# Kernel tuning notes

Measured on AMD Instinct MI355X. Metric: run time of the kernel, lower is better.

Reference implementation:

```python
import jax, jax.numpy as jnp
import numpy as np
from jax import lax

DN = ('NCHW', 'OIHW', 'NCHW')


def _conv(x, w, b, stride, pad):
    y = lax.conv_general_dilated(x, w, (stride, stride), [(pad, pad), (pad, pad)],
                                 dimension_numbers=DN)
    return y + b[None, :, None, None]


def _deconv(x, w, b, stride, pad):
    # torch ConvTranspose2d weight: (in, out, kH, kW). Equivalent forward conv:
    # flip spatially, swap in/out, dilate input by stride, pad by k-1-pad.
    k = w.shape[2]
    kern = jnp.flip(w, (2, 3)).transpose(1, 0, 2, 3)  # (out, in, kH, kW)
    p = k - 1 - pad
    y = lax.conv_general_dilated(x, kern, (1, 1), [(p, p), (p, p)],
                                 lhs_dilation=(stride, stride), dimension_numbers=DN)
    return y + b[None, :, None, None]


def setup_inputs() -> dict:
    key = jax.random.key(0)
    ks = jax.random.split(key, 16)
    s = 0.05
    D, K, H = 64, 512, 128  # embedding_dim, num_embeddings, hidden_channels
    inp = {
        'x': jax.random.uniform(ks[0], (16, 3, 256, 256), dtype=jnp.float32),
        'conv1_w': jax.random.normal(ks[1], (H, 3, 4, 4), jnp.float32) * s,
        'conv1_b': jnp.zeros((H,), jnp.float32),
        'conv2_w': jax.random.normal(ks[2], (H, H, 4, 4), jnp.float32) * s,
        'conv2_b': jnp.zeros((H,), jnp.float32),
        'conv3_w': jax.random.normal(ks[3], (D, H, 3, 3), jnp.float32) * s,
        'conv3_b': jnp.zeros((D,), jnp.float32),
        'emb': jax.random.normal(ks[4], (K, D), jnp.float32),
        'deconv1_w': jax.random.normal(ks[5], (D, H, 4, 4), jnp.float32) * s,
        'deconv1_b': jnp.zeros((H,), jnp.float32),
        'deconv2_w': jax.random.normal(ks[6], (H, H, 4, 4), jnp.float32) * s,
        'deconv2_b': jnp.zeros((H,), jnp.float32),
        'deconv3_w': jax.random.normal(ks[7], (H, 3, 3, 3), jnp.float32) * s,
        'deconv3_b': jnp.zeros((3,), jnp.float32),
    }
    return inp


def reference(x, conv1_w, conv1_b, conv2_w, conv2_b, conv3_w, conv3_b, emb,
              deconv1_w, deconv1_b, deconv2_w, deconv2_b, deconv3_w, deconv3_b):
    # Encoder
    h = jax.nn.relu(_conv(x, conv1_w, conv1_b, 2, 1))
    h = jax.nn.relu(_conv(h, conv2_w, conv2_b, 2, 1))
    z_e = _conv(h, conv3_w, conv3_b, 1, 1)  # (B, 64, 64, 64)

    # Vector quantizer (faithful to torch: flatten NCHW directly to (-1, D))
    D = emb.shape[1]
    flat = z_e.reshape(-1, D)  # (N, D)
    d = (jnp.sum(flat * flat, axis=1, keepdims=True)
         + jnp.sum(emb * emb, axis=1)
         - 2.0 * flat @ emb.T)  # (N, K)
    indices = jnp.argmin(d, axis=1)[:, None]  # (N, 1)
    z_q = emb[indices[:, 0]].reshape(z_e.shape)

    # Decoder
    g = jax.nn.relu(_deconv(z_q, deconv1_w, deconv1_b, 2, 1))
    g = jax.nn.relu(_deconv(g, deconv2_w, deconv2_b, 2, 1))
    x_recon = jax.nn.sigmoid(_deconv(g, deconv3_w, deconv3_b, 1, 1))
    return (x_recon, indices, z_q)
```

## Files before the change

kernel.cpp:

```cpp
#include <hip/hip_runtime.h>
#include <hip/hip_bf16.h>

#define DEV __device__ __forceinline__

typedef __attribute__((ext_vector_type(8))) short bf16x8;
typedef __attribute__((ext_vector_type(4))) float f32x4;
typedef __attribute__((ext_vector_type(4))) unsigned short u16x4;

#define MFMA16(a,b,c) __builtin_amdgcn_mfma_f32_16x16x32_bf16(a,b,c,0,0,0)

DEV unsigned short bfbits(float v){ __hip_bfloat16 h = __float2bfloat16(v); return *(unsigned short*)&h; }
DEV float bf2f(unsigned short u){ __hip_bfloat16 h = *(__hip_bfloat16*)&u; return __bfloat162float(h); }
DEV void split3(float v, unsigned short& h, unsigned short& m, unsigned short& l) {
  h = bfbits(v);        float r  = v - bf2f(h);
  m = bfbits(r);        float r2 = r - bf2f(m);
  l = bfbits(r2);
}
DEV uint4 zero4(){ uint4 z; z.x=0; z.y=0; z.z=0; z.w=0; return z; }
DEV void gload_lds16(const void* g, void* l) {
  __builtin_amdgcn_global_load_lds(
      (const __attribute__((address_space(1))) void*)g,
      (__attribute__((address_space(3))) void*)l, 16, 0, 0);
}

DEV void prep_deconv_img(int i, int CI, const float* __restrict__ w, unsigned short* __restrict__ w2) {
  const int nch = CI/16;
  int cil = i & 7, s = (i >> 3) & 7, co = (i >> 6) & 127, f = (i >> 13) & 1;
  int rest = i >> 14;
  int ch = rest % nch, e = rest / nch;
  int k = ch*64 + s*8 + cil;
  int ci = (k & 15) | ((k >> 6) << 4);
  int tap = (k >> 4) & 3, a = tap >> 1, b = tap & 1;
  float v = w[ (((long)ci*128 + co)*4 + (2*a+1-e))*4 + (2*b+1-f) ];
  w2[(long)(e*nch + ch)*16384 + ((long)(f*128 + co))*64 + ((s ^ (co&7))*8) + cil] = bfbits(v);
}
__global__ __launch_bounds__(256) void wprep_all(
    const float* __restrict__ c1w, float* __restrict__ w2c1,
    const float* __restrict__ c2w, unsigned short* __restrict__ w2c2,
    const float* __restrict__ c3w, unsigned short* __restrict__ w2c3,
    const float* __restrict__ d1w, unsigned short* __restrict__ w2d1,
    const float* __restrict__ d2w, unsigned short* __restrict__ w2d2,
    const float* __restrict__ d3w, unsigned short* __restrict__ w2d3,
    const float* __restrict__ emb, float* __restrict__ esq) {
  const int bx = blockIdx.x, t = threadIdx.x;
  if (bx < 24) {
    int i = bx*256 + t;
    if (i < 6144) {
      int tap = i & 15, ci = (i>>4) % 3, co = i / 48;
      w2c1[((long)ci*16 + tap)*128 + co] = c1w[i];
    }
  } else if (bx < 1048) {
    int i = (bx-24)*256 + t;
    int cil = i & 7, s = (i>>3) & 15, co = (i>>7) & 63;
    int ch = (i>>13) & 15, cog = i >> 17;
    int co_g = cog*64 + co, ci = ch*8 + cil, ky = s >> 2, kx = s & 3;
    float v = c2w[(((long)co_g*128 + ci)*4 + ky)*4 + kx];
    unsigned short h,m,l; split3(v,h,m,l);
    long base = (long)(cog*16 + ch)*24576 + ((long)co*16 + (s ^ (co&15)))*8 + cil;
    w2c2[base] = h; w2c2[base + 8192] = m; w2c2[base + 16384] = l;
  } else if (bx < 1432) {
    int i = (bx-1048)*256 + t;
    int k = i % 1536, co = i / 1536;
    int ch = k / 96, rem = k % 96;
    int tap = rem >> 3, cil = rem & 7;
    int ci = ch*8 + cil, ky = tap >> 2, kx = tap & 3;
    float v = (kx < 3) ? c3w[(((long)co*128 + ci)*3 + ky)*3 + kx] : 0.f;
    unsigned short h,m,l; split3(v,h,m,l);
    long base = (long)ch*24576 + ((long)co*16 + (tap ^ (co&15)))*8 + cil;
    w2c3[base] = h; w2c3[base + 8192] = m; w2c3[base + 16384] = l;
  } else if (bx < 1944) {
    prep_deconv_img((bx-1432)*256 + t, 64, d1w, w2d1);
  } else if (bx < 2968) {
    prep_deconv_img((bx-1944)*256 + t, 128, d2w, w2d2);
  } else if (bx < 3064) {
    int i = (bx-2968)*256 + t;
    if (i < 24576) {
      int k = i % 1536, co = i / 1536;
      int ch = k / 96, rem = k % 96;
      int tap = rem >> 3, cil = rem & 7;
      int ci = ch*8 + cil, ky = tap >> 2, kx = tap & 3;
      float v = (co < 3 && kx < 3) ? d3w[(((long)ci*3 + co)*3 + ky)*3 + kx] : 0.f;
      w2d3[i] = bfbits(v);
    }
  } else {
    int code = (bx-3064)*256 + t;
    if (code < 512) {
      const float4* ev = (const float4*)(emb + (long)code*64);
      float s = 0.f;
      #pragma unroll
      for (int q=0;q<16;q++){ float4 e4 = ev[q];
        s += e4.x*e4.x + e4.y*e4.y + e4.z*e4.z + e4.w*e4.w; }
      esq[code] = s;
    }
  }
}

__global__ __launch_bounds__(256) void conv1_split(
    const float* __restrict__ x, const float* __restrict__ w2,
    const float* __restrict__ bias, unsigned short* __restrict__ h1, long PS1) {
  __shared__ __align__(16) float sIn[3][18][20];
  __shared__ __align__(16) float sW[3*16*64];
  const int tid = threadIdx.x;
  const int b = blockIdx.z >> 1, cog = blockIdx.z & 1;
  const int co0 = cog*64;
  const int oy0 = blockIdx.y*8, ox0 = blockIdx.x*8;
  const int cg2 = tid >> 5;
  const int pg2 = tid & 31;
  const int r = pg2 >> 2, pxp = (pg2 & 3)*2;
  float acc[8][2];
  #pragma unroll
  for (int c=0;c<8;c++){ float bv = bias[co0 + cg2*8 + c];
    acc[c][0]=bv; acc[c][1]=bv; }
  const float* xb = x + (long)b*3*256*256;
  const int iy0 = 2*oy0 - 1, ix0 = 2*ox0 - 1;
  for (int t=tid; t<3*18*18; t+=256) {
    int xx = t%18, yy=(t/18)%18, ci=t/324;
    int gy = iy0+yy, gx = ix0+xx;
    float v = 0.f;
    if (gy>=0 && gy<256 && gx>=0 && gx<256) v = xb[((long)ci*256+gy)*256+gx];
    sIn[ci][yy][xx] = v;
  }
  for (int t=tid; t<3*16*64; t+=256) {
    sW[t] = w2[(long)(t>>6)*128 + co0 + (t&63)];
  }
  __syncthreads();
  for (int ci=0; ci<3; ci++) {
    #pragma unroll
    for (int ky=0;ky<4;ky++)
    #pragma unroll
    for (int kx=0;kx<4;kx++) {
      const float* wp = &sW[(ci*16 + ky*4+kx)*64 + cg2*8];
      float4 w0 = *(const float4*)wp;
      float4 w1 = *(const float4*)(wp+4);
      const int yy = 2*r + ky;
      #pragma unroll
      for (int p=0;p<2;p++) {
        float iv = sIn[ci][yy][2*(pxp+p)+kx];
        acc[0][p] += w0.x*iv; acc[1][p] += w0.y*iv;
        acc[2][p] += w0.z*iv; acc[3][p] += w0.w*iv;
        acc[4][p] += w1.x*iv; acc[5][p] += w1.y*iv;
        acc[6][p] += w1.z*iv; acc[7][p] += w1.w*iv;
      }
    }
  }
  const int chg = cog*8 + cg2;
  #pragma unroll
  for (int p=0;p<2;p++) {
    unsigned short th[8], tm[8], tl[8];
    #pragma unroll
    for (int c=0;c<8;c++) {
      float v = fmaxf(acc[c][p], 0.f);
      split3(v, th[c], tm[c], tl[c]);
    }
    long base = (((long)(b*128 + oy0+r)*16 + chg)*128 + ox0+pxp+p)*8;
    *(uint4*)(h1 + base)          = *(uint4*)th;
    *(uint4*)(h1 + PS1 + base)    = *(uint4*)tm;
    *(uint4*)(h1 + 2*PS1 + base)  = *(uint4*)tl;
  }
}

__global__ __launch_bounds__(256, 2) void conv2_mfma(
    const unsigned short* __restrict__ h1, long PS1,
    const unsigned short* __restrict__ w2,
    const float* __restrict__ bias,
    unsigned short* __restrict__ h2I) {
  __shared__ __align__(16) unsigned short sA[3][4][130][8];
  __shared__ __align__(16) unsigned short sB[24576];
  const int tid = threadIdx.x;
  const int oy = blockIdx.x, cog = blockIdx.y, b = blockIdx.z;
  const int wave = tid >> 6, lane = tid & 63;
  const int wr = wave >> 1, wc = wave & 1;
  const int col_l = lane & 15, kg = lane >> 4;
  const int iy0 = 2*oy - 1;
  f32x4 acc[2][2] = {};
  unsigned short* sAf = &sA[0][0][0][0];
  const unsigned short* bsrc = w2 + (long)cog*16*24576;

  long aOff[6]; int aLdsO[6]; bool aOk[6];
  #pragma unroll
  for (int j = 0; j < 6; ++j) {
    int idx = tid + j*256;
    int px = idx & 127, rr = (idx >> 7) & 3, pl = idx >> 9;
    int iy = iy0 + rr;
    aOk[j] = (iy >= 0 && iy < 128);
    aOff[j] = (long)pl*PS1 + (long)(b*128 + (aOk[j]?iy:0))*16384 + px*8;
    aLdsO[j] = ((pl*4 + rr)*130 + px + 1)*8;
  }
  uint4 pA[6];
  #pragma unroll
  for (int j=0;j<6;j++)  pA[j] = aOk[j] ? *(const uint4*)(h1 + aOff[j]) : zero4();

  if (tid < 24) {
    int pl = tid>>3, rr=(tid>>1)&3, c=tid&1;
    *(uint4*)&sA[pl][rr][c?129:0][0] = zero4();
  }

  for (int ch = 0; ch < 16; ++ch) {
    __syncthreads();
    #pragma unroll
    for (int j=0;j<6;j++)  *(uint4*)(sAf + aLdsO[j]) = pA[j];
    #pragma unroll
    for (int j = 0; j < 12; ++j) {
      int blk = wave*12 + j;
      gload_lds16(bsrc + (long)ch*24576 + blk*512 + lane*8, &sB[blk*512]);
    }
    __syncthreads();
    if (ch < 15) {
      #pragma unroll
      for (int j=0;j<6;j++)  pA[j] = aOk[j] ? *(const uint4*)(h1 + aOff[j] + (ch+1)*1024) : zero4();
      __builtin_amdgcn_sched_barrier(0);
    }
    #pragma unroll
    for (int s = 0; s < 4; ++s) {
      bf16x8 aF[2][3]; bf16x8 bF[2][3];
      const int tap = s*4 + kg;
      #pragma unroll
      for (int mf = 0; mf < 2; ++mf) {
        int ox = wr*32 + mf*16 + col_l;
        #pragma unroll
        for (int pl = 0; pl < 3; ++pl)
          aF[mf][pl] = *(const bf16x8*)&sA[pl][s][2*ox + kg][0];
      }
      #pragma unroll
      for (int nf = 0; nf < 2; ++nf) {
        int co = wc*32 + nf*16 + col_l;
        int ba = (co*16 + (tap ^ (co&15)))*8;
        bF[nf][0] = *(const bf16x8*)&sB[ba];
        bF[nf][1] = *(const bf16x8*)&sB[ba + 8192];
        bF[nf][2] = *(const bf16x8*)&sB[ba + 16384];
      }
      __builtin_amdgcn_s_setprio(1);
      #pragma unroll
      for (int mf = 0; mf < 2; ++mf)
      #pragma unroll
      for (int nf = 0; nf < 2; ++nf) {
        f32x4 a = acc[mf][nf];
        a = MFMA16(aF[mf][0], bF[nf][0], a);
        a = MFMA16(aF[mf][0], bF[nf][1], a);
        a = MFMA16(aF[mf][1], bF[nf][0], a);
        a = MFMA16(aF[mf][0], bF[nf][2], a);
        a = MFMA16(aF[mf][2], bF[nf][0], a);
        a = MFMA16(aF[mf][1], bF[nf][1], a);
        acc[mf][nf] = a;
      }
      __builtin_amdgcn_s_setprio(0);
    }
  }
  __syncthreads();
  #pragma unroll
  for (int nf = 0; nf < 2; ++nf) {
    int co = wc*32 + nf*16 + col_l;
    float bv = bias[cog*64 + co];
    #pragma unroll
    for (int mf = 0; mf < 2; ++mf) {
      int px0 = wr*32 + mf*16 + kg*4;
      u16x4 oh, om, ol;
      #pragma unroll
      for (int r = 0; r < 4; ++r) {
        float v = fmaxf(acc[mf][nf][r] + bv, 0.f);
        unsigned short h,m,l; split3(v,h,m,l);
        oh[r]=h; om[r]=m; ol[r]=l;
      }
      *(u16x4*)&sB[(0*64 + co)*72 + px0] = oh;
      *(u16x4*)&sB[(1*64 + co)*72 + px0] = om;
      *(u16x4*)&sB[(2*64 + co)*72 + px0] = ol;
    }
  }
  __syncthreads();
  #pragma unroll
  for (int j = 0; j < 6; ++j) {
    int idx = tid + j*256;
    int pl = idx >> 9, ch = (idx >> 6) & 7, px = idx & 63;
    unsigned short tmp[8];
    #pragma unroll
    for (int c = 0; c < 8; ++c) tmp[c] = sB[(pl*64 + ch*8 + c)*72 + px];
    *(uint4*)(h2I + ((((long)(b*64 + oy)*3 + pl)*16 + cog*8 + ch)*64 + px)*8) = *(uint4*)tmp;
  }
}

__global__ __launch_bounds__(256, 2) void conv3_mfma(
    const unsigned short* __restrict__ h2I,
    const unsigned short* __restrict__ w2,
    const float* __restrict__ bias,
    unsigned short* __restrict__ zeH, unsigned short* __restrict__ zeM,
    unsigned short* __restrict__ zeL) {
  __shared__ __align__(16) unsigned short sA3[3][3][68][8];
  __shared__ __align__(16) unsigned short sB[24576];
  const int tid = threadIdx.x;
  const int oy = blockIdx.x, b = blockIdx.z;
  const int wave = tid >> 6, lane = tid & 63;
  const int wr = wave >> 1, wc = wave & 1;
  const int col_l = lane & 15, kg = lane >> 4;
  f32x4 acc[2][2] = {};
  if (tid < 27) {
    int row = tid/3, c = tid%3;
    int pl = row/3, rr = row%3;
    *(uint4*)&sA3[pl][rr][(c==0)?0:(64+c)][0] = zero4();
  }
  if (oy == 0 && tid < 192) {
    int pl = tid >> 6, px = tid & 63;
    *(uint4*)&sA3[pl][0][px+1][0] = zero4();
  }
  if (oy == 63 && tid < 192) {
    int pl = tid >> 6, px = tid & 63;
    *(uint4*)&sA3[pl][2][px+1][0] = zero4();
  }

  for (int ch = 0; ch < 16; ++ch) {
    __syncthreads();
    #pragma unroll
    for (int j = 0; j < 3; ++j) {
      int row = wave*3 + j;
      if (row < 9) {
        int pl = row/3, rr = row%3;
        int iy = oy + rr - 1;
        if (iy >= 0 && iy < 64)
          gload_lds16(h2I + ((((long)(b*64 + iy)*3 + pl)*16 + ch)*64)*8 + lane*8,
                      &sA3[pl][rr][1][0]);
      }
    }
    #pragma unroll
    for (int j = 0; j < 12; ++j) {
      int blk = wave*12 + j;
      gload_lds16(w2 + (long)ch*24576 + blk*512 + lane*8, &sB[blk*512]);
    }
    __syncthreads();
    #pragma unroll
    for (int s = 0; s < 3; ++s) {
      bf16x8 aF[2][3]; bf16x8 bF[2][3];
      const int tap = s*4 + kg;
      #pragma unroll
      for (int mf = 0; mf < 2; ++mf) {
        int ox = wr*32 + mf*16 + col_l;
        #pragma unroll
        for (int pl = 0; pl < 3; ++pl)
          aF[mf][pl] = *(const bf16x8*)&sA3[pl][s][ox + kg][0];
      }
      #pragma unroll
      for (int nf = 0; nf < 2; ++nf) {
        int co = wc*32 + nf*16 + col_l;
        int ba = (co*16 + (tap ^ (co&15)))*8;
        bF[nf][0] = *(const bf16x8*)&sB[ba];
        bF[nf][1] = *(const bf16x8*)&sB[ba + 8192];
        bF[nf][2] = *(const bf16x8*)&sB[ba + 16384];
      }
      __builtin_amdgcn_s_setprio(1);
      #pragma unroll
      for (int mf = 0; mf < 2; ++mf)
      #pragma unroll
      for (int nf = 0; nf < 2; ++nf) {
        f32x4 a = acc[mf][nf];
        a = MFMA16(aF[mf][0], bF[nf][0], a);
        a = MFMA16(aF[mf][0], bF[nf][1], a);
        a = MFMA16(aF[mf][1], bF[nf][0], a);
        a = MFMA16(aF[mf][0], bF[nf][2], a);
        a = MFMA16(aF[mf][2], bF[nf][0], a);
        a = MFMA16(aF[mf][1], bF[nf][1], a);
        acc[mf][nf] = a;
      }
      __builtin_amdgcn_s_setprio(0);
    }
  }
  __syncthreads();
  #pragma unroll
  for (int nf = 0; nf < 2; ++nf) {
    int co = wc*32 + nf*16 + col_l;
    float bv = bias[co];
    #pragma unroll
    for (int mf = 0; mf < 2; ++mf) {
      int px0 = wr*32 + mf*16 + kg*4;
      u16x4 oh, om, ol;
      #pragma unroll
      for (int r = 0; r < 4; ++r) {
        float v = acc[mf][nf][r] + bv;
        unsigned short h,m,l; split3(v,h,m,l);
        oh[r]=h; om[r]=m; ol[r]=l;
      }
      *(u16x4*)&sB[(0*64 + co)*72 + px0] = oh;
      *(u16x4*)&sB[(1*64 + co)*72 + px0] = om;
      *(u16x4*)&sB[(2*64 + co)*72 + px0] = ol;
    }
  }
  __syncthreads();
  #pragma unroll
  for (int j = 0; j < 6; ++j) {
    int idx = tid + j*256;
    int pl = idx >> 9, co_l = (idx >> 3) & 63, q = idx & 7;
    uint4 v = *(const uint4*)&sB[(pl*64 + co_l)*72 + q*8];
    unsigned short* dst = (pl==0) ? zeH : ((pl==1) ? zeM : zeL);
    *(uint4*)(dst + ((long)(b*64 + co_l)*64 + oy)*64 + q*8) = v;
  }
}

template<int TX, int MODE>
struct SmemD {
  union {
    struct { __align__(16) unsigned short In[2][TX+2][24];
             __align__(16) unsigned short W[2*128*64]; } o;
    struct { __align__(16) unsigned short In[2][TX+2][16];
             __align__(16) unsigned short W[2*128*64]; } v;
    __align__(16) unsigned short Out[128][136];
  };
};

template<int CIN, int TX, int MODE>
__global__ __launch_bounds__(TX*4, (TX==64)?3:4) void deconv_mfma(
    const void* __restrict__ xin, const unsigned short* __restrict__ w2,
    const float* __restrict__ bias, unsigned short* __restrict__ yI) {
  constexpr int NTHR = TX*4;
  constexpr int NWAVE = NTHR/64;
  constexpr int NWG  = 32/NWAVE;
  __shared__ SmemD<TX,MODE> sm;
  unsigned short* Wb = MODE ? &sm.v.W[0] : &sm.o.W[0];

  const int tid = threadIdx.x;
  const int ty = blockIdx.x, e = blockIdx.y, b = blockIdx.z;
  const int wave = tid >> 6, lane = tid & 63;
  const int wc = wave & 1, wr = wave >> 1;
  const int f = (wr*64) / TX;
  const int tx_base = (wr*64) & (TX-1);
  const int col_l = lane & 15, kg = lane >> 4;
  const unsigned short* wsrc = w2 + (long)e*(CIN/16)*16384;

  constexpr int TPR = NTHR/32;
  const int rowid = tid / TPR, liO = tid % TPR;
  const int sci = rowid >> 1, srr = rowid & 1;
  float4 pLo, pHi; uint4 pIn;
  long aBase = 0; bool aOk = false;
  int pxV = 0, halfV = 0, rrV = 0;
  if (MODE == 0) {
    int iy = ty + e - 1 + srr;
    aOk = (iy >= 0 && iy < TX);
    aBase = ((long)b*CIN + sci)*TX*TX + (long)(aOk?iy:0)*TX + liO*8;
    if (aOk) { const float4* s4 = (const float4*)((const float*)xin + aBase);
               pLo = s4[0]; pHi = s4[1]; }
  } else {
    halfV = tid & 1; pxV = (tid >> 1) & (TX-1); rrV = tid >> 8;
    int iy = ty + e - 1 + rrV;
    aOk = (iy >= 0 && iy < TX);
    aBase = ((long)b*TX + (aOk?iy:0))*((long)(CIN/8)*TX*8) + (long)halfV*TX*8 + pxV*8;
    pIn = aOk ? *(const uint4*)((const unsigned short*)xin + aBase) : zero4();
  }

  if (MODE == 0) {
    if (tid < 64) {
      int rr = tid & 1, cc = ((tid>>1)&1) ? TX+1 : 0, ci = tid >> 2;
      sm.o.In[rr][cc][ci] = 0;
    }
  } else {
    if (tid < 8) {
      int rr = tid & 1, c = (tid>>1)&1, hf = (tid>>2)&1;
      *(uint4*)&sm.v.In[rr][c?TX+1:0][hf*8] = zero4();
    }
  }

  f32x4 acc[4][4] = {};
  for (int ch = 0; ch < CIN/16; ++ch) {
    __syncthreads();
    if (MODE == 0) {
      unsigned short vals[8];
      if (aOk) {
        float4 lo = pLo, hi = pHi;
        vals[0]=bfbits(lo.x); vals[1]=bfbits(lo.y); vals[2]=bfbits(lo.z); vals[3]=bfbits(lo.w);
        vals[4]=bfbits(hi.x); vals[5]=bfbits(hi.y); vals[6]=bfbits(hi.z); vals[7]=bfbits(hi.w);
      } else {
        #pragma unroll
        for (int j=0;j<8;j++) vals[j] = 0;
      }
      #pragma unroll
      for (int j=0;j<8;j++) {
        int jj = (j + liO) & 7;
        sm.o.In[srr][1 + liO*8 + jj][sci] = vals[jj];
      }
    } else {
      *(uint4*)&sm.v.In[rrV][pxV+1][halfV*8] = pIn;
    }
    #pragma unroll
    for (int j = 0; j < NWG; ++j) {
      int blk = wave*NWG + j;
      gload_lds16(wsrc + (long)ch*16384 + blk*512 + lane*8, Wb + blk*512);
    }
    __syncthreads();
    if (ch + 1 < CIN/16) {
      if (MODE == 0) {
        if (aOk) { const float4* s4 = (const float4*)((const float*)xin + aBase + (long)(ch+1)*16*TX*TX);
                   pLo = s4[0]; pHi = s4[1]; }
      } else {
        pIn = aOk ? *(const uint4*)((const unsigned short*)xin + aBase + (ch+1)*2*TX*8) : zero4();
      }
      __builtin_amdgcn_sched_barrier(0);
    }
    #pragma unroll
    for (int kk = 0; kk < 2; ++kk) {
      bf16x8 aF[4];
      const int tap = kk*2 + (kg >> 1), a = tap >> 1, bb = tap & 1;
      #pragma unroll
      for (int mf = 0; mf < 4; ++mf) {
        int tx = tx_base + mf*16 + col_l;
        if (MODE == 0) aF[mf] = *(const bf16x8*)&sm.o.In[1-a][tx + 1 + f - bb][(kg&1)*8];
        else           aF[mf] = *(const bf16x8*)&sm.v.In[1-a][tx + 1 + f - bb][(kg&1)*8];
      }
      const int slot = kk*4 + kg;
      __builtin_amdgcn_s_setprio(1);
      #pragma unroll
      for (int nf = 0; nf < 4; ++nf) {
        int co_l = nf*16 + col_l;
        bf16x8 bF = *(const bf16x8*)(Wb + (f*128 + wc*64 + co_l)*64 + (slot ^ (co_l & 7))*8);
        #pragma unroll
        for (int mf = 0; mf < 4; ++mf)
          acc[mf][nf] = MFMA16(aF[mf], bF, acc[mf][nf]);
      }
      __builtin_amdgcn_s_setprio(0);
    }
  }

  __syncthreads();
  float bv[4];
  #pragma unroll
  for (int nf = 0; nf < 4; ++nf) bv[nf] = bias[wc*64 + nf*16 + col_l];
  const int oy = 2*ty + e;
  if constexpr (TX == 64) {
    #pragma unroll
    for (int mf = 0; mf < 4; ++mf)
    #pragma unroll
    for (int nf = 0; nf < 4; ++nf) {
      int co = wc*64 + nf*16 + col_l;
      #pragma unroll
      for (int r = 0; r < 4; ++r) {
        int tx = tx_base + mf*16 + kg*4 + r;
        float v = fmaxf(acc[mf][nf][r] + bv[nf], 0.f);
        int ox = 2*tx + f;
        sm.Out[ox][co ^ (((ox>>3)&7)<<3)] = bfbits(v);
      }
    }
    __syncthreads();
    #pragma unroll
    for (int j = 0; j < 8; ++j) {
      int i = tid + j*NTHR;
      int px = i & 127, chn = i >> 7;
      uint4 vv = *(const uint4*)&sm.Out[px][(chn*8) ^ (((px>>3)&7)<<3)];
      *(uint4*)(yI + ((((long)b*128 + oy)*16 + chn)*128 + px)*8) = vv;
    }
  } else {
    const int myp = wr & 1;
    #pragma unroll
    for (int p = 0; p < 2; ++p) {
      if (myp == p) {
        #pragma unroll
        for (int mf = 0; mf < 4; ++mf)
        #pragma unroll
        for (int nf = 0; nf < 4; ++nf) {
          int co = wc*64 + nf*16 + col_l;
          #pragma unroll
          for (int r = 0; r < 4; ++r) {
            int tx = tx_base + mf*16 + kg*4 + r;
            float v = fmaxf(acc[mf][nf][r] + bv[nf], 0.f);
            int ox = 2*tx + f;
            sm.Out[ox & 127][co ^ (((ox>>3)&7)<<3)] = bfbits(v);
          }
        }
      }
      __syncthreads();
      #pragma unroll
      for (int j = 0; j < 4; ++j) {
        int i = tid + j*NTHR;
        int px = i & 127, chn = i >> 7;
        uint4 vv = *(const uint4*)&sm.Out[px][(chn*8) ^ (((px>>3)&7)<<3)];
        int pxg = p*128 + px;
        *(uint4*)(yI + ((((long)b*256 + oy)*16 + chn)*256 + pxg)*8) = vv;
      }
      if (p == 0) __syncthreads();
    }
  }
}

__global__ __launch_bounds__(512, 4) void deconv3_mfma(
    const unsigned short* __restrict__ g2I,
    const unsigned short* __restrict__ w2,
    const float* __restrict__ bias, float* __restrict__ y) {
  __shared__ __align__(16) unsigned short sA[4][260][8];
  __shared__ __align__(16) unsigned short sB[16*12*16*8];
  const int tid = threadIdx.x;
  const int oy0 = blockIdx.x*2, b = blockIdx.y;
  const int wave = tid >> 6, lane = tid & 63;
  const int col_l = lane & 15, kg = lane >> 4;
  const int r = wave >> 2;
  const int pxb = (wave & 3)*64;
  for (int i = tid; i < 3072; i += 512) {
    int co = i & 15, tap = (i>>4) % 12, ch = i/192;
    *(uint4*)&sB[((ch*12+tap)*16+co)*8] = *(const uint4*)(w2 + (long)co*1536 + ch*96 + tap*8);
  }
  if (tid < 16) {
    int dy = tid >> 2, c = tid & 3;
    *(uint4*)&sA[dy][(c<2)?c:(256+c)][0] = zero4();
  }
  long aBase[2]; int aLdsO[2]; bool aOk[2];
  #pragma unroll
  for (int u = 0; u < 2; ++u) {
    int idx = tid + u*512;
    int px = idx & 255, dy = idx >> 8;
    int iy = oy0 - 1 + dy;
    aOk[u] = (iy >= 0 && iy < 256);
    aBase[u] = ((long)(b*256 + (aOk[u]?iy:0)))*32768 + px*8;
    aLdsO[u] = (dy*260 + px + 2)*8;
  }
  uint4 pA[2];
  #pragma unroll
  for (int u=0;u<2;u++) pA[u] = aOk[u] ? *(const uint4*)(g2I + aBase[u]) : zero4();

  unsigned short* sAf = &sA[0][0][0];
  f32x4 acc[4] = {};
  for (int ch = 0; ch < 16; ++ch) {
    __syncthreads();
    #pragma unroll
    for (int u=0;u<2;u++) *(uint4*)(sAf + aLdsO[u]) = pA[u];
    __syncthreads();
    if (ch < 15) {
      #pragma unroll
      for (int u=0;u<2;u++)
        pA[u] = aOk[u] ? *(const uint4*)(g2I + aBase[u] + (ch+1)*2048) : zero4();
      __builtin_amdgcn_sched_barrier(0);
    }
    #pragma unroll
    for (int s = 0; s < 3; ++s) {
      bf16x8 bF = *(const bf16x8*)&sB[((ch*12 + s*4 + kg)*16 + col_l)*8];
      __builtin_amdgcn_s_setprio(1);
      #pragma unroll
      for (int mf = 0; mf < 4; ++mf) {
        int px = pxb + mf*16 + col_l;
        bf16x8 aF = *(const bf16x8*)&sA[r + 2 - s][px + 3 - kg][0];
        acc[mf] = MFMA16(aF, bF, acc[mf]);
      }
      __builtin_amdgcn_s_setprio(0);
    }
  }
  if (col_l < 3) {
    const int oy = oy0 + r;
    float bv = bias[col_l];
    #pragma unroll
    for (int mf = 0; mf < 4; ++mf) {
      int px = pxb + mf*16 + kg*4;
      float4 o;
      o.x = 1.f/(1.f + expf(-(acc[mf][0] + bv)));
      o.y = 1.f/(1.f + expf(-(acc[mf][1] + bv)));
      o.z = 1.f/(1.f + expf(-(acc[mf][2] + bv)));
      o.w = 1.f/(1.f + expf(-(acc[mf][3] + bv)));
      *(float4*)(y + ((long)(b*3 + col_l)*256 + oy)*256 + px) = o;
    }
  }
}

__global__ __launch_bounds__(256, 2) void vq_mfma(
    const unsigned short* __restrict__ zeH, const unsigned short* __restrict__ zeM,
    const unsigned short* __restrict__ zeL,
    const float* __restrict__ emb, const float* __restrict__ esq,
    float* __restrict__ out_idx, float* __restrict__ zq) {
  __shared__ __align__(16) unsigned short sA[64*3*8*8];
  __shared__ __align__(16) unsigned short sB[128*3*8*8];
  __shared__ float snb[128];
  __shared__ int sidx[64];
  const int tid = threadIdx.x;
  const long n0 = (long)blockIdx.x*64;
  const int wave = tid >> 6, lane = tid & 63;
  const int col = lane & 15, kg = lane >> 4;

  #pragma unroll
  for (int j = 0; j < 6; ++j) {
    int idx = tid + j*256;
    int pl = idx >> 9, rem = idx & 511;
    int n = rem >> 3, slot = rem & 7;
    const unsigned short* src = (pl==0 ? zeH : (pl==1 ? zeM : zeL)) + (n0+n)*64 + slot*8;
    *(uint4*)&sA[((n*3 + pl)*8 + (slot ^ (n&7)))*8] = *(const uint4*)src;
  }

  const int codeT = tid >> 1, halfT = tid & 1;
  float4 pB[8];
  #pragma unroll
  for (int q = 0; q < 8; ++q)
    pB[q] = *(const float4*)(emb + (long)codeT*64 + halfT*32 + q*4);
  float pSn = (tid < 128) ? esq[tid] : 0.f;

  float best[4] = {3.4e38f,3.4e38f,3.4e38f,3.4e38f};
  int bidx[4] = {0,0,0,0};

  for (int ch = 0; ch < 4; ++ch) {
    __syncthreads();
    #pragma unroll
    for (int s4 = 0; s4 < 4; ++s4) {
      int slot = halfT*4 + s4;
      float4 lo = pB[s4*2], hi = pB[s4*2+1];
      unsigned short th[8], tm[8], tl[8];
      split3(lo.x, th[0], tm[0], tl[0]); split3(lo.y, th[1], tm[1], tl[1]);
      split3(lo.z, th[2], tm[2], tl[2]); split3(lo.w, th[3], tm[3], tl[3]);
      split3(hi.x, th[4], tm[4], tl[4]); split3(hi.y, th[5], tm[5], tl[5]);
      split3(hi.z, th[6], tm[6], tl[6]); split3(hi.w, th[7], tm[7], tl[7]);
      int base = ((codeT*3)*8 + (slot ^ (codeT&7)))*8;
      *(uint4*)&sB[base]       = *(uint4*)th;
      *(uint4*)&sB[base + 64]  = *(uint4*)tm;
      *(uint4*)&sB[base + 128] = *(uint4*)tl;
    }
    if (tid < 128) snb[tid] = pSn;
    if (ch < 3) {
      #pragma unroll
      for (int q = 0; q < 8; ++q)
        pB[q] = *(const float4*)(emb + ((long)(ch+1)*128 + codeT)*64 + halfT*32 + q*4);
      if (tid < 128) pSn = esq[(ch+1)*128 + tid];
    }
    __syncthreads();

    f32x4 acc[8] = {};
    #pragma unroll
    for (int kk = 0; kk < 2; ++kk) {
      const int nloc = wave*16 + col;
      const int slot = kk*4 + kg;
      bf16x8 aF[3];
      #pragma unroll
      for (int pl = 0; pl < 3; ++pl)
        aF[pl] = *(const bf16x8*)&sA[((nloc*3 + pl)*8 + (slot ^ (nloc&7)))*8];
      __builtin_amdgcn_s_setprio(1);
      #pragma unroll
      for (int cf = 0; cf < 8; ++cf) {
        int cl = cf*16 + col;
        int bb = ((cl*3)*8 + (slot ^ (cl&7)))*8;
        bf16x8 b0 = *(const bf16x8*)&sB[bb];
        bf16x8 b1 = *(const bf16x8*)&sB[bb + 64];
        bf16x8 b2 = *(const bf16x8*)&sB[bb + 128];
        f32x4 a = acc[cf];
        a = MFMA16(aF[0], b0, a);
        a = MFMA16(aF[0], b1, a);
        a = MFMA16(aF[1], b0, a);
        a = MFMA16(aF[0], b2, a);
        a = MFMA16(aF[2], b0, a);
        a = MFMA16(aF[1], b1, a);
        acc[cf] = a;
      }
      __builtin_amdgcn_s_setprio(0);
    }
    #pragma unroll
    for (int cf = 0; cf < 8; ++cf) {
      float sv = snb[cf*16 + col];
      int code = ch*128 + cf*16 + col;
      #pragma unroll
      for (int j = 0; j < 4; ++j) {
        float s = sv - 2.f*acc[cf][j];
        if (s < best[j]) { best[j] = s; bidx[j] = code; }
      }
    }
  }

  #pragma unroll
  for (int j = 0; j < 4; ++j) {
    float b = best[j]; int ii = bidx[j];
    #pragma unroll
    for (int off = 1; off < 16; off <<= 1) {
      float ob = __shfl_xor(b, off);
      int oi = __shfl_xor(ii, off);
      if (ob < b || (ob == b && oi < ii)) { b = ob; ii = oi; }
    }
    if (col == 0) sidx[wave*16 + kg*4 + j] = ii;
  }
  __syncthreads();
  if (tid < 64) out_idx[n0 + tid] = (float)sidx[tid];
  #pragma unroll
  for (int j = 0; j < 4; ++j) {
    int t = tid + j*256;
    int row = t >> 4, q = t & 15;
    float4 v = *(const float4*)(emb + (long)sidx[row]*64 + q*4);
    *(float4*)(zq + (n0 + row)*64 + q*4) = v;
  }
}

extern "C" void kernel_launch(void* const* d_in, const int* in_sizes, int n_in,
                              void* d_out, int out_size, void* d_ws, size_t ws_size,
                              hipStream_t stream) {
  const float* x   = (const float*)d_in[0];
  const float* c1w = (const float*)d_in[1];  const float* c1b = (const float*)d_in[2];
  const float* c2w = (const float*)d_in[3];  const float* c2b = (const float*)d_in[4];
  const float* c3w = (const float*)d_in[5];  const float* c3b = (const float*)d_in[6];
  const float* emb = (const float*)d_in[7];
  const float* d1w = (const float*)d_in[8];  const float* d1b = (const float*)d_in[9];
  const float* d2w = (const float*)d_in[10]; const float* d2b = (const float*)d_in[11];
  const float* d3w = (const float*)d_in[12]; const float* d3b = (const float*)d_in[13];
  float* out = (float*)d_out;

  float* xrec = out;
  float* oidx = out + 3145728;
  float* zq   = out + 3211264;

  const long XB  = 196608;
  const long ZEB = 262144;
  const long H2B = 1572864;

  const size_t NEEDED   = 112273408ULL;
  const size_t NEEDED8  = 170994688ULL;
  const size_t NEEDED16 = 288434176ULL;
  if (ws_size < NEEDED) return;
  const bool use16 = (ws_size >= NEEDED16);
  const bool use8  = (ws_size >= NEEDED8);
  char* wsb = (char*)d_ws;

  unsigned short* zeL = (unsigned short*)out;

  if (use16) {
    unsigned short* h1  = (unsigned short*)wsb;
    unsigned short* h2I = (unsigned short*)(wsb + 201326592);
    unsigned short* zeH = (unsigned short*)(wsb + 251658240);
    unsigned short* zeM = (unsigned short*)(wsb + 268435456);
    char* W = wsb + 285212672;
    float* w2c1          = (float*)(W);
    unsigned short* w2c2 = (unsigned short*)(W + 24576);
    unsigned short* w2c3 = (unsigned short*)(W + 1597440);
    unsigned short* w2d1 = (unsigned short*)(W + 2383872);
    unsigned short* w2d2 = (unsigned short*)(W + 2646016);
    unsigned short* w2d3 = (unsigned short*)(W + 3170304);
    float* esq           = (float*)(W + 3219456);

    wprep_all<<<3066, 256, 0, stream>>>(c1w, w2c1, c2w, w2c2, c3w, w2c3,
                                        d1w, w2d1, d2w, w2d2, d3w, w2d3, emb, esq);
    conv1_split<<<dim3(16,16,32), 256, 0, stream>>>(x, w2c1, c1b, h1, 33554432L);
    conv2_mfma<<<dim3(64,2,16), 256, 0, stream>>>(h1, 33554432L, w2c2, c2b, h2I);
    conv3_mfma<<<dim3(64,1,16), 256, 0, stream>>>(h2I, w2c3, c3b, zeH, zeM, zeL);
    vq_mfma<<<1024, 256, 0, stream>>>(zeH, zeM, zeL, emb, esq, oidx, zq);

    unsigned short* g2g = (unsigned short*)wsb;
    unsigned short* g1g = (unsigned short*)(wsb + 134217728);
    for (int g = 0; g < 2; ++g) {
      deconv_mfma<64, 64, 0 ><<<dim3(64, 2, 8), 256, 0, stream>>>(
          (const void*)(zq + (long)g*8*ZEB), w2d1, d1b, g1g);
      deconv_mfma<128,128,1 ><<<dim3(128,2,8), 512, 0, stream>>>(
          (const void*)g1g, w2d2, d2b, g2g);
      deconv3_mfma<<<dim3(128,8), 512, 0, stream>>>(
          g2g, w2d3, d3b, xrec + (long)g*8*XB);
    }
    return;
  }

  unsigned short* h1grp = (unsigned short*)wsb;
  unsigned short* h2I   = (unsigned short*)(wsb + 67108864);
  unsigned short* zeH = (unsigned short*)(wsb + 92274688);
  unsigned short* zeM = (unsigned short*)(wsb + 100663296);
  char* W = use8 ? (wsb + 167772160) : (wsb + 109051904);
  float* w2c1          = (float*)(W);
  unsigned short* w2c2 = (unsigned short*)(W + 24576);
  unsigned short* w2c3 = (unsigned short*)(W + 1597440);
  unsigned short* w2d1 = (unsigned short*)(W + 2383872);
  unsigned short* w2d2 = (unsigned short*)(W + 2646016);
  unsigned short* w2d3 = (unsigned short*)(W + 3170304);
  float* esq           = (float*)(W + 3219456);

  wprep_all<<<3066, 256, 0, stream>>>(c1w, w2c1, c2w, w2c2, c3w, w2c3,
                                      d1w, w2d1, d2w, w2d2, d3w, w2d3, emb, esq);

  const long PS1 = 8388608;
  for (int g = 0; g < 4; ++g) {
    conv1_split<<<dim3(16,16,8), 256, 0, stream>>>(
        x + (long)g*4*XB, w2c1, c1b, h1grp, PS1);
    conv2_mfma<<<dim3(64,2,4), 256, 0, stream>>>(
        h1grp, PS1, w2c2, c2b, h2I + (long)(g&1)*4*H2B);
    if (g & 1) {
      long zo = (long)(g>>1)*8*ZEB;
      conv3_mfma<<<dim3(64,1,8), 256, 0, stream>>>(
          h2I, w2c3, c3b, zeH + zo, zeM + zo, zeL + zo);
    }
  }
  vq_mfma<<<1024, 256, 0, stream>>>(zeH, zeM, zeL, emb, esq, oidx, zq);

  if (use8) {
    unsigned short* g2g = (unsigned short*)wsb;
    unsigned short* g1g = (unsigned short*)(wsb + 134217728);
    for (int g = 0; g < 2; ++g) {
      deconv_mfma<64, 64, 0 ><<<dim3(64, 2, 8), 256, 0, stream>>>(
          (const void*)(zq + (long)g*8*ZEB), w2d1, d1b, g1g);
      deconv_mfma<128,128,1 ><<<dim3(128,2,8), 512, 0, stream>>>(
          (const void*)g1g, w2d2, d2b, g2g);
      deconv3_mfma<<<dim3(128,8), 512, 0, stream>>>(
          g2g, w2d3, d3b, xrec + (long)g*8*XB);
    }
  } else {
    unsigned short* g2g = (unsigned short*)wsb;
    unsigned short* g1g = (unsigned short*)(wsb + 67108864);
    for (int g = 0; g < 4; ++g) {
      deconv_mfma<64, 64, 0 ><<<dim3(64, 2, 4), 256, 0, stream>>>(
          (const void*)(zq + (long)g*4*ZEB), w2d1, d1b, g1g);
      deconv_mfma<128,128,1 ><<<dim3(128,2,4), 512, 0, stream>>>(
          (const void*)g1g, w2d2, d2b, g2g);
      deconv3_mfma<<<dim3(128,4), 512, 0, stream>>>(
          g2g, w2d3, d3b, xrec + (long)g*4*XB);
    }
  }
}
```

Baseline: 670.9 us.

## Add software-pipelined deconv2 kernel with double-buffered LDS weights and inputs

Replaces the generic templated deconv_mfma used for the second transposed convolution with a dedicated kernel. The new kernel prefetches the next channel chunk's input rows into registers and the next weight slab into a second LDS buffer via global_load_lds while MFMAs run on the current one. It also uses explicit waitcnt, barriers and setprio so that loads overlap with compute. The aim is to hide global-memory latency in the largest decoder stage, at the cost of more LDS and hand-tuned synchronisation that could be fragile.

```diff
diff --git a/kernel.cpp b/kernel.cpp
--- a/kernel.cpp
+++ b/kernel.cpp
@@ -574,6 +574,121 @@
   }
 }
 
+__global__ __launch_bounds__(512, 4) void deconv2_pipe(
+    const unsigned short* __restrict__ xin,
+    const unsigned short* __restrict__ w2,
+    const float* __restrict__ bias, unsigned short* __restrict__ yI) {
+  __shared__ union {
+    struct { __align__(16) unsigned short In[2][130][16];
+             __align__(16) unsigned short W[2][16384]; } s;
+    __align__(16) unsigned short Out[128][136];
+  } sm;
+  const int tid = threadIdx.x;
+  const int ty = blockIdx.x, e = blockIdx.y, b = blockIdx.z;
+  const int wave = tid >> 6, lane = tid & 63;
+  const int wc = wave & 1, wr = wave >> 1;
+  const int f = (wr*64) >> 7;
+  const int tx_base = (wr*64) & 127;
+  const int col_l = lane & 15, kg = lane >> 4;
+  const unsigned short* wsrc = w2 + (long)e*8*16384;
+
+  const int halfV = tid & 1, pxV = (tid >> 1) & 127, rrV = tid >> 8;
+  const int iyA = ty + e - 1 + rrV;
+  const bool aOk = (iyA >= 0 && iyA < 128);
+  const long aBase = ((long)b*128 + (aOk?iyA:0))*16384 + (long)halfV*1024 + pxV*8;
+  uint4 pIn = aOk ? *(const uint4*)(xin + aBase) : zero4();
+
+  if (tid < 8) {
+    int rr = tid & 1, c = (tid>>1)&1, hf = (tid>>2)&1;
+    *(uint4*)&sm.s.In[rr][c?129:0][hf*8] = zero4();
+  }
+  #pragma unroll
+  for (int j = 0; j < 4; ++j) {
+    int blk = wave*4 + j;
+    gload_lds16(wsrc + blk*512 + lane*8, &sm.s.W[0][blk*512]);
+  }
+
+  f32x4 acc[4][4] = {};
+  int cur = 0;
+  for (int ch = 0; ch < 8; ++ch) {
+    asm volatile("s_waitcnt lgkmcnt(0)" ::: "memory");
+    __builtin_amdgcn_s_barrier();
+    *(uint4*)&sm.s.In[rrV][pxV+1][halfV*8] = pIn;
+    if (ch < 7) {
+      pIn = aOk ? *(const uint4*)(xin + aBase + (ch+1)*2048) : zero4();
+      #pragma unroll
+      for (int j = 0; j < 4; ++j) {
+        int blk = wave*4 + j;
+        gload_lds16(wsrc + (long)(ch+1)*16384 + blk*512 + lane*8, &sm.s.W[cur^1][blk*512]);
+      }
+      asm volatile("s_waitcnt vmcnt(5)" ::: "memory");
+    } else {
+      asm volatile("s_waitcnt vmcnt(0)" ::: "memory");
+    }
+    asm volatile("s_waitcnt lgkmcnt(0)" ::: "memory");
+    __builtin_amdgcn_s_barrier();
+    __builtin_amdgcn_sched_barrier(0);
+    const unsigned short* Wb = &sm.s.W[cur][0];
+    #pragma unroll
+    for (int kk = 0; kk < 2; ++kk) {
+      bf16x8 aF[4];
+      const int tap = kk*2 + (kg >> 1), a = tap >> 1, bb = tap & 1;
+      #pragma unroll
+      for (int mf = 0; mf < 4; ++mf) {
+        int tx = tx_base + mf*16 + col_l;
+        aF[mf] = *(const bf16x8*)&sm.s.In[1-a][tx + 1 + f - bb][(kg&1)*8];
+      }
+      const int slot = kk*4 + kg;
+      __builtin_amdgcn_s_setprio(1);
+      #pragma unroll
+      for (int nf = 0; nf < 4; ++nf) {
+        int co_l = nf*16 + col_l;
+        bf16x8 bF = *(const bf16x8*)(Wb + (f*128 + wc*64 + co_l)*64 + (slot ^ (co_l & 7))*8);
+        #pragma unroll
+        for (int mf = 0; mf < 4; ++mf)
+          acc[mf][nf] = MFMA16(aF[mf], bF, acc[mf][nf]);
+      }
+      __builtin_amdgcn_s_setprio(0);
+    }
+    cur ^= 1;
+  }
+
+  __syncthreads();
+  float bv[4];
+  #pragma unroll
+  for (int nf = 0; nf < 4; ++nf) bv[nf] = bias[wc*64 + nf*16 + col_l];
+  const int oy = 2*ty + e;
+  const int myp = wr & 1;
+  #pragma unroll
+  for (int p = 0; p < 2; ++p) {
+    if (myp == p) {
+      #pragma unroll
+      for (int mf = 0; mf < 4; ++mf)
+      #pragma unroll
+      for (int nf = 0; nf < 4; ++nf) {
+        int co = wc*64 + nf*16 + col_l;
+        #pragma unroll
+        for (int r = 0; r < 4; ++r) {
+          int tx = tx_base + mf*16 + kg*4 + r;
+          float v = fmaxf(acc[mf][nf][r] + bv[nf], 0.f);
+          int ox = 2*tx + f;
+          sm.Out[ox & 127][co ^ (((ox>>3)&7)<<3)] = bfbits(v);
+        }
+      }
+    }
+    __syncthreads();
+    #pragma unroll
+    for (int j = 0; j < 4; ++j) {
+      int i = tid + j*512;
+      int px = i & 127, chn = i >> 7;
+      uint4 vv = *(const uint4*)&sm.Out[px][(chn*8) ^ (((px>>3)&7)<<3)];
+      int pxg = p*128 + px;
+      *(uint4*)(yI + ((((long)b*256 + oy)*16 + chn)*256 + pxg)*8) = vv;
+    }
+    if (p == 0) __syncthreads();
+  }
+}
+
 __global__ __launch_bounds__(512, 4) void deconv3_mfma(
     const unsigned short* __restrict__ g2I,
     const unsigned short* __restrict__ w2,
@@ -827,8 +942,7 @@
     for (int g = 0; g < 2; ++g) {
       deconv_mfma<64, 64, 0 ><<<dim3(64, 2, 8), 256, 0, stream>>>(
           (const void*)(zq + (long)g*8*ZEB), w2d1, d1b, g1g);
-      deconv_mfma<128,128,1 ><<<dim3(128,2,8), 512, 0, stream>>>(
-          (const void*)g1g, w2d2, d2b, g2g);
+      deconv2_pipe<<<dim3(128,2,8), 512, 0, stream>>>(g1g, w2d2, d2b, g2g);
       deconv3_mfma<<<dim3(128,8), 512, 0, stream>>>(
           g2g, w2d3, d3b, xrec + (long)g*8*XB);
     }
@@ -871,8 +985,7 @@
     for (int g = 0; g < 2; ++g) {
       deconv_mfma<64, 64, 0 ><<<dim3(64, 2, 8), 256, 0, stream>>>(
           (const void*)(zq + (long)g*8*ZEB), w2d1, d1b, g1g);
-      deconv_mfma<128,128,1 ><<<dim3(128,2,8), 512, 0, stream>>>(
-          (const void*)g1g, w2d2, d2b, g2g);
+      deconv2_pipe<<<dim3(128,2,8), 512, 0, stream>>>(g1g, w2d2, d2b, g2g);
       deconv3_mfma<<<dim3(128,8), 512, 0, stream>>>(
           g2g, w2d3, d3b, xrec + (long)g*8*XB);
     }
@@ -882,8 +995,7 @@
     for (int g = 0; g < 4; ++g) {
       deconv_mfma<64, 64, 0 ><<<dim3(64, 2, 4), 256, 0, stream>>>(
           (const void*)(zq + (long)g*4*ZEB), w2d1, d1b, g1g);
-      deconv_mfma<128,128,1 ><<<dim3(128,2,4), 512, 0, stream>>>(
-          (const void*)g1g, w2d2, d2b, g2g);
+      deconv2_pipe<<<dim3(128,2,4), 512, 0, stream>>>(g1g, w2d2, d2b, g2g);
       deconv3_mfma<<<dim3(128,4), 512, 0, stream>>>(
           g2g, w2d3, d3b, xrec + (long)g*4*XB);
     }
```

Result: no change. 668.5 us (-0.3%).
